# Optimization experiments

Hardware: AMD Instinct MI355X
Metric: run time of the kernel (lower is better)

Reference implementation:

```python
import jax, jax.numpy as jnp
import numpy as np

TIME_STEPS = 49      # time_steps init arg
NUM_STEPS = 5000     # (time_steps+1)/dt = max_solve_steps
DT = 0.01            # dt0 in diffeqsolve
B = 8192             # batch of independent simulations


def setup_inputs() -> dict:
    key = jax.random.key(0)
    k1, k2, k3 = jax.random.split(key, 3)
    # positive, well-conditioned rates in [0.05, 0.5)
    condition = 0.05 + 0.45 * jax.random.uniform(k1, (B, 4), dtype=jnp.float32)
    # standard normals; scaled by sqrt(dt) inside reference -> Brownian increments
    dW = jax.random.normal(k2, (NUM_STEPS, B), dtype=jnp.float32)
    # uniform jitter used in summarize()'s max_at
    u = jax.random.uniform(k3, (B,), dtype=jnp.float32)
    return {"condition": condition, "dW": dW, "u": u}


def _simulate(condition, dW):
    # condition columns: infection_rate, recovery_rate, r0_mean_reversion, r0_volatility
    inf_rate = condition[:, 0]
    rec = condition[:, 1]
    mr = condition[:, 2]
    vol = condition[:, 3]
    r0_init = inf_rate / rec
    b = condition.shape[0]
    y0 = jnp.stack([
        jnp.full((b,), 0.99, condition.dtype),  # S
        jnp.full((b,), 0.01, condition.dtype),  # I
        jnp.zeros((b,), condition.dtype),       # R
        r0_init,                                # R0
    ], axis=-1)  # [B,4]
    sqrt_dt = jnp.sqrt(jnp.asarray(DT, condition.dtype))

    def step(y, dw):
        s, i, r, r0 = y[:, 0], y[:, 1], y[:, 2], y[:, 3]
        newly_infected = r0 * rec * s
        newly_recovered = rec * i
        # Euler-Maruyama: drift * dt + diffusion * dW, diffusion only on R0,
        # scaled by sqrt(|R0|) as in sde()
        y_new = jnp.stack([
            s - DT * newly_infected,
            i + DT * (newly_infected - newly_recovered),
            r + DT * newly_recovered,
            r0 + DT * mr * (r0_init - r0) + jnp.sqrt(jnp.abs(r0)) * vol * (dw * sqrt_dt),
        ], axis=-1)
        return y_new, y_new[:, 1]  # carry full state, emit infected fraction

    _, infected = jax.lax.scan(step, y0, dW)  # infected: [NUM_STEPS, B]
    # SaveAt ts = 1..TIME_STEPS: step k ends at t=(k+1)*DT, so t=m is index 100*m-1
    x = infected[99:100 * TIME_STEPS:100]  # [TIME_STEPS, B]
    return jnp.nan_to_num(x, nan=0.0, posinf=0.0, neginf=0.0)


def reference(condition, dW, u):
    x = _simulate(condition, dW)          # [T, B] infected trajectories
    x = jnp.clip(x, 1e-5)
    max_ = x.max(axis=0)
    max_at = (jnp.argmax(x, axis=0).astype(x.dtype) + u) / TIME_STEPS
    vol = jnp.std(jnp.diff(jnp.log(x), axis=0), axis=0)
    return jnp.stack([max_, max_at, vol], axis=-1)  # [B, 3]
```

## Files before the change

kernel.cpp:

```cpp
#include <hip/hip_runtime.h>
#include <math.h>

#define BATCH 8192
#define TPB   32
#define SEG   50


#define REP50(M) M(0) M(1) M(2) M(3) M(4) M(5) M(6) M(7) M(8) M(9) \
  M(10) M(11) M(12) M(13) M(14) M(15) M(16) M(17) M(18) M(19) \
  M(20) M(21) M(22) M(23) M(24) M(25) M(26) M(27) M(28) M(29) \
  M(30) M(31) M(32) M(33) M(34) M(35) M(36) M(37) M(38) M(39) \
  M(40) M(41) M(42) M(43) M(44) M(45) M(46) M(47) M(48) M(49)

#define DECL_A(k) float A##k = 0.0f;
#define DECL_B(k) float B##k = 0.0f;

#define LDL(k) "global_load_dword %[d" #k "], %[ob], %[sb]\n\t" \
               "v_add_u32 %[ob], 0x8000, %[ob]\n\t"

#define LD25 LDL(0) LDL(1) LDL(2) LDL(3) LDL(4) LDL(5) LDL(6) LDL(7) \
  LDL(8) LDL(9) LDL(10) LDL(11) LDL(12) LDL(13) LDL(14) LDL(15) LDL(16) \
  LDL(17) LDL(18) LDL(19) LDL(20) LDL(21) LDL(22) LDL(23) LDL(24)

#define LOAD_LO(P) asm volatile(LD25 \
  : [d0]"=v"(P##0),[d1]"=v"(P##1),[d2]"=v"(P##2),[d3]"=v"(P##3), \
    [d4]"=v"(P##4),[d5]"=v"(P##5),[d6]"=v"(P##6),[d7]"=v"(P##7), \
    [d8]"=v"(P##8),[d9]"=v"(P##9),[d10]"=v"(P##10),[d11]"=v"(P##11), \
    [d12]"=v"(P##12),[d13]"=v"(P##13),[d14]"=v"(P##14),[d15]"=v"(P##15), \
    [d16]"=v"(P##16),[d17]"=v"(P##17),[d18]"=v"(P##18),[d19]"=v"(P##19), \
    [d20]"=v"(P##20),[d21]"=v"(P##21),[d22]"=v"(P##22),[d23]"=v"(P##23), \
    [d24]"=v"(P##24),[ob]"+v"(ob) \
  : [sb]"s"(dWp))

#define LOAD_HI(P) asm volatile(LD25 \
  : [d0]"=v"(P##25),[d1]"=v"(P##26),[d2]"=v"(P##27),[d3]"=v"(P##28), \
    [d4]"=v"(P##29),[d5]"=v"(P##30),[d6]"=v"(P##31),[d7]"=v"(P##32), \
    [d8]"=v"(P##33),[d9]"=v"(P##34),[d10]"=v"(P##35),[d11]"=v"(P##36), \
    [d12]"=v"(P##37),[d13]"=v"(P##38),[d14]"=v"(P##39),[d15]"=v"(P##40), \
    [d16]"=v"(P##41),[d17]"=v"(P##42),[d18]"=v"(P##43),[d19]"=v"(P##44), \
    [d20]"=v"(P##45),[d21]"=v"(P##46),[d22]"=v"(P##47),[d23]"=v"(P##48), \
    [d24]"=v"(P##49),[ob]"+v"(ob) \
  : [sb]"s"(dWp))

#define WAIT_LO(P) asm volatile("s_waitcnt vmcnt(50)" \
  : "+v"(P##0),"+v"(P##1),"+v"(P##2),"+v"(P##3),"+v"(P##4), \
    "+v"(P##5),"+v"(P##6),"+v"(P##7),"+v"(P##8),"+v"(P##9), \
    "+v"(P##10),"+v"(P##11),"+v"(P##12),"+v"(P##13),"+v"(P##14), \
    "+v"(P##15),"+v"(P##16),"+v"(P##17),"+v"(P##18),"+v"(P##19), \
    "+v"(P##20),"+v"(P##21),"+v"(P##22),"+v"(P##23),"+v"(P##24))

#define WAIT_HI(P) asm volatile("s_waitcnt vmcnt(50)" \
  : "+v"(P##25),"+v"(P##26),"+v"(P##27),"+v"(P##28),"+v"(P##29), \
    "+v"(P##30),"+v"(P##31),"+v"(P##32),"+v"(P##33),"+v"(P##34), \
    "+v"(P##35),"+v"(P##36),"+v"(P##37),"+v"(P##38),"+v"(P##39), \
    "+v"(P##40),"+v"(P##41),"+v"(P##42),"+v"(P##43),"+v"(P##44), \
    "+v"(P##45),"+v"(P##46),"+v"(P##47),"+v"(P##48),"+v"(P##49))

#define STEP_BODY(dwv) { \
    float dw  = (dwv); \
    float pr  = dtrec * r0; \
    float ps  = pr * s; \
    float r0a = r0 * c1 + c2; \
    float sq  = sqrtf(fabsf(r0)); \
    float g   = dw * volc; \
    s  = s - ps; \
    i_ = i_ * ci + ps; \
    r0 = r0a + sq * g; }

#define STEP_A(k) STEP_BODY(A##k)
#define STEP_B(k) STEP_BODY(B##k)

__global__ __attribute__((amdgpu_flat_work_group_size(TPB, TPB),
                          amdgpu_waves_per_eu(1, 1)))
void sir_sde_kernel(const float* __restrict__ cond,
                    const float* __restrict__ dW,
                    const float* __restrict__ uu,
                    float* __restrict__ out)
{
    const int b = blockIdx.x * TPB + threadIdx.x;

    const float u_in     = uu[b];
    const float inf_rate = cond[b * 4 + 0];
    const float rec      = cond[b * 4 + 1];
    const float mr       = cond[b * 4 + 2];
    const float vol      = cond[b * 4 + 3];

    const float dt    = 0.01f;
    const float r0i   = inf_rate / rec;
    const float dtrec = dt * rec;
    const float ci    = 1.0f - dtrec;
    const float c1    = 1.0f - dt * mr;
    const float c2    = (dt * mr) * r0i;
    const float volc  = vol * sqrtf(dt);

    float s  = 0.99f;
    float i_ = 0.01f;
    float r0 = r0i;

    float maxv = -1.0f, maxat = 0.0f;
    float prevlx = 0.0f, sum = 0.0f, sumsq = 0.0f;
    int   reccount = 0;

    REP50(DECL_A)
    REP50(DECL_B)

    const float* dWp = dW;
    unsigned ob = (unsigned)b * 4u;

    LOAD_LO(A); LOAD_HI(A);

#pragma clang loop unroll(disable)
    for (int sg = 0; sg < 98; sg += 2) {
        LOAD_LO(B); LOAD_HI(B);

        WAIT_LO(A); WAIT_HI(A);
        REP50(STEP_A)

        LOAD_LO(A); LOAD_HI(A);

        WAIT_LO(B); WAIT_HI(B);
        REP50(STEP_B)

        {
            float x = __builtin_isfinite(i_) ? i_ : 0.0f;
            x = fmaxf(x, 1e-5f);
            float lx = logf(x);
            if (reccount > 0) {
                float d = lx - prevlx;
                sum   += d;
                sumsq += d * d;
            }
            prevlx = lx;
            if (x > maxv) { maxv = x; maxat = (float)reccount; }
            ++reccount;
        }
    }

    asm volatile("s_waitcnt vmcnt(0)"
      : "+v"(A0),"+v"(A1),"+v"(A2),"+v"(A3),"+v"(A4),"+v"(A5),"+v"(A6),
        "+v"(A7),"+v"(A8),"+v"(A9),"+v"(A10),"+v"(A11),"+v"(A12),"+v"(A13),
        "+v"(A14),"+v"(A15),"+v"(A16),"+v"(A17),"+v"(A18),"+v"(A19),
        "+v"(A20),"+v"(A21),"+v"(A22),"+v"(A23),"+v"(A24) : : "memory");
    asm volatile("s_waitcnt vmcnt(0)"
      : "+v"(A25),"+v"(A26),"+v"(A27),"+v"(A28),"+v"(A29),"+v"(A30),
        "+v"(A31),"+v"(A32),"+v"(A33),"+v"(A34),"+v"(A35),"+v"(A36),
        "+v"(A37),"+v"(A38),"+v"(A39),"+v"(A40),"+v"(A41),"+v"(A42),
        "+v"(A43),"+v"(A44),"+v"(A45),"+v"(A46),"+v"(A47),"+v"(A48),
        "+v"(A49) : : "memory");

    float mean = sum / 48.0f;
    float var  = sumsq / 48.0f - mean * mean;
    var = fmaxf(var, 0.0f);
    float volout    = sqrtf(var);
    float maxat_out = (maxat + u_in) / 49.0f;

    out[b * 3 + 0] = maxv;
    out[b * 3 + 1] = maxat_out;
    out[b * 3 + 2] = volout;
}

extern "C" void kernel_launch(void* const* d_in, const int* in_sizes, int n_in,
                              void* d_out, int out_size, void* d_ws, size_t ws_size,
                              hipStream_t stream)
{
    (void)in_sizes; (void)n_in; (void)out_size; (void)d_ws; (void)ws_size;
    const float* cond = (const float*)d_in[0];
    const float* dW   = (const float*)d_in[1];
    const float* uu   = (const float*)d_in[2];
    float* out = (float*)d_out;

    dim3 grid(BATCH / TPB), block(TPB);
    hipLaunchKernelGGL(sir_sde_kernel, grid, block, 0, stream, cond, dW, uu, out);
}
```

Baseline: 566.8 us.

## Pre-transpose dW into per-block contiguous tiles before the simulation kernel

Adds a reshuffle kernel that rearranges the first 4900 noise rows into a workspace so that each 32-lane block's 50-step segment is one contiguous 6.4KB chunk. The simulation kernel can then use immediate offsets on a fixed lane offset instead of strided 32KB-apart row loads. The aim is better DRAM and TLB locality for the many tiny strided loads. The cost is an extra full read and write pass over about 78MB of dW plus a second launch. The old direct kernel is kept as a fallback when the workspace is too small.

Measured after the change: 613.5 us. 8.2% more time.

```diff
diff --git a/kernel.cpp b/kernel.cpp
--- a/kernel.cpp
+++ b/kernel.cpp
@@ -15,14 +15,60 @@
 #define DECL_A(k) float A##k = 0.0f;
 #define DECL_B(k) float B##k = 0.0f;
 
+#define LD25OFF \
+  "global_load_dword %[d0], %[vo], %[sb]\n\t" \
+  "global_load_dword %[d1], %[vo], %[sb] offset:128\n\t" \
+  "global_load_dword %[d2], %[vo], %[sb] offset:256\n\t" \
+  "global_load_dword %[d3], %[vo], %[sb] offset:384\n\t" \
+  "global_load_dword %[d4], %[vo], %[sb] offset:512\n\t" \
+  "global_load_dword %[d5], %[vo], %[sb] offset:640\n\t" \
+  "global_load_dword %[d6], %[vo], %[sb] offset:768\n\t" \
+  "global_load_dword %[d7], %[vo], %[sb] offset:896\n\t" \
+  "global_load_dword %[d8], %[vo], %[sb] offset:1024\n\t" \
+  "global_load_dword %[d9], %[vo], %[sb] offset:1152\n\t" \
+  "global_load_dword %[d10], %[vo], %[sb] offset:1280\n\t" \
+  "global_load_dword %[d11], %[vo], %[sb] offset:1408\n\t" \
+  "global_load_dword %[d12], %[vo], %[sb] offset:1536\n\t" \
+  "global_load_dword %[d13], %[vo], %[sb] offset:1664\n\t" \
+  "global_load_dword %[d14], %[vo], %[sb] offset:1792\n\t" \
+  "global_load_dword %[d15], %[vo], %[sb] offset:1920\n\t" \
+  "global_load_dword %[d16], %[vo], %[sb] offset:2048\n\t" \
+  "global_load_dword %[d17], %[vo], %[sb] offset:2176\n\t" \
+  "global_load_dword %[d18], %[vo], %[sb] offset:2304\n\t" \
+  "global_load_dword %[d19], %[vo], %[sb] offset:2432\n\t" \
+  "global_load_dword %[d20], %[vo], %[sb] offset:2560\n\t" \
+  "global_load_dword %[d21], %[vo], %[sb] offset:2688\n\t" \
+  "global_load_dword %[d22], %[vo], %[sb] offset:2816\n\t" \
+  "global_load_dword %[d23], %[vo], %[sb] offset:2944\n\t" \
+  "global_load_dword %[d24], %[vo], %[sb] offset:3072"
+
+#define LOAD_LO(P, ptr) asm volatile(LD25OFF \
+  : [d0]"=v"(P##0),[d1]"=v"(P##1),[d2]"=v"(P##2),[d3]"=v"(P##3), \
+    [d4]"=v"(P##4),[d5]"=v"(P##5),[d6]"=v"(P##6),[d7]"=v"(P##7), \
+    [d8]"=v"(P##8),[d9]"=v"(P##9),[d10]"=v"(P##10),[d11]"=v"(P##11), \
+    [d12]"=v"(P##12),[d13]"=v"(P##13),[d14]"=v"(P##14),[d15]"=v"(P##15), \
+    [d16]"=v"(P##16),[d17]"=v"(P##17),[d18]"=v"(P##18),[d19]"=v"(P##19), \
+    [d20]"=v"(P##20),[d21]"=v"(P##21),[d22]"=v"(P##22),[d23]"=v"(P##23), \
+    [d24]"=v"(P##24) \
+  : [vo]"v"(vlane), [sb]"s"(ptr))
+
+#define LOAD_HI(P, ptr) asm volatile(LD25OFF \
+  : [d0]"=v"(P##25),[d1]"=v"(P##26),[d2]"=v"(P##27),[d3]"=v"(P##28), \
+    [d4]"=v"(P##29),[d5]"=v"(P##30),[d6]"=v"(P##31),[d7]"=v"(P##32), \
+    [d8]"=v"(P##33),[d9]"=v"(P##34),[d10]"=v"(P##35),[d11]"=v"(P##36), \
+    [d12]"=v"(P##37),[d13]"=v"(P##38),[d14]"=v"(P##39),[d15]"=v"(P##40), \
+    [d16]"=v"(P##41),[d17]"=v"(P##42),[d18]"=v"(P##43),[d19]"=v"(P##44), \
+    [d20]"=v"(P##45),[d21]"=v"(P##46),[d22]"=v"(P##47),[d23]"=v"(P##48), \
+    [d24]"=v"(P##49) \
+  : [vo]"v"(vlane), [sb]"s"(ptr))
+
 #define LDL(k) "global_load_dword %[d" #k "], %[ob], %[sb]\n\t" \
                "v_add_u32 %[ob], 0x8000, %[ob]\n\t"
-
-#define LD25 LDL(0) LDL(1) LDL(2) LDL(3) LDL(4) LDL(5) LDL(6) LDL(7) \
+#define LD25B LDL(0) LDL(1) LDL(2) LDL(3) LDL(4) LDL(5) LDL(6) LDL(7) \
   LDL(8) LDL(9) LDL(10) LDL(11) LDL(12) LDL(13) LDL(14) LDL(15) LDL(16) \
   LDL(17) LDL(18) LDL(19) LDL(20) LDL(21) LDL(22) LDL(23) LDL(24)
 
-#define LOAD_LO(P) asm volatile(LD25 \
+#define LOADD_LO(P) asm volatile(LD25B \
   : [d0]"=v"(P##0),[d1]"=v"(P##1),[d2]"=v"(P##2),[d3]"=v"(P##3), \
     [d4]"=v"(P##4),[d5]"=v"(P##5),[d6]"=v"(P##6),[d7]"=v"(P##7), \
     [d8]"=v"(P##8),[d9]"=v"(P##9),[d10]"=v"(P##10),[d11]"=v"(P##11), \
@@ -31,8 +77,7 @@
     [d20]"=v"(P##20),[d21]"=v"(P##21),[d22]"=v"(P##22),[d23]"=v"(P##23), \
     [d24]"=v"(P##24),[ob]"+v"(ob) \
   : [sb]"s"(dWp))
-
-#define LOAD_HI(P) asm volatile(LD25 \
+#define LOADD_HI(P) asm volatile(LD25B \
   : [d0]"=v"(P##25),[d1]"=v"(P##26),[d2]"=v"(P##27),[d3]"=v"(P##28), \
     [d4]"=v"(P##29),[d5]"=v"(P##30),[d6]"=v"(P##31),[d7]"=v"(P##32), \
     [d8]"=v"(P##33),[d9]"=v"(P##34),[d10]"=v"(P##35),[d11]"=v"(P##36), \
@@ -48,7 +93,6 @@
     "+v"(P##10),"+v"(P##11),"+v"(P##12),"+v"(P##13),"+v"(P##14), \
     "+v"(P##15),"+v"(P##16),"+v"(P##17),"+v"(P##18),"+v"(P##19), \
     "+v"(P##20),"+v"(P##21),"+v"(P##22),"+v"(P##23),"+v"(P##24))
-
 #define WAIT_HI(P) asm volatile("s_waitcnt vmcnt(50)" \
   : "+v"(P##25),"+v"(P##26),"+v"(P##27),"+v"(P##28),"+v"(P##29), \
     "+v"(P##30),"+v"(P##31),"+v"(P##32),"+v"(P##33),"+v"(P##34), \
@@ -70,105 +114,155 @@
 #define STEP_A(k) STEP_BODY(A##k)
 #define STEP_B(k) STEP_BODY(B##k)
 
+#define SIM_PROLOG \
+    const int bx = blockIdx.x; \
+    const int lane = threadIdx.x; \
+    const int b = bx * TPB + lane; \
+    const float u_in     = uu[b]; \
+    const float inf_rate = cond[b * 4 + 0]; \
+    const float rec      = cond[b * 4 + 1]; \
+    const float mr       = cond[b * 4 + 2]; \
+    const float vol      = cond[b * 4 + 3]; \
+    const float dt    = 0.01f; \
+    const float r0i   = inf_rate / rec; \
+    const float dtrec = dt * rec; \
+    const float ci    = 1.0f - dtrec; \
+    const float c1    = 1.0f - dt * mr; \
+    const float c2    = (dt * mr) * r0i; \
+    const float volc  = vol * sqrtf(dt); \
+    float s  = 0.99f; \
+    float i_ = 0.01f; \
+    float r0 = r0i; \
+    float maxv = -1.0f, maxat = 0.0f; \
+    float prevlx = 0.0f, sum = 0.0f, sumsq = 0.0f; \
+    int   reccount = 0; \
+    REP50(DECL_A) \
+    REP50(DECL_B)
+
+#define RECORD_BLOCK { \
+    float x = __builtin_isfinite(i_) ? i_ : 0.0f; \
+    x = fmaxf(x, 1e-5f); \
+    float lx = logf(x); \
+    if (reccount > 0) { float d = lx - prevlx; sum += d; sumsq += d * d; } \
+    prevlx = lx; \
+    if (x > maxv) { maxv = x; maxat = (float)reccount; } \
+    ++reccount; }
+
+#define SIM_EPILOG \
+    asm volatile("s_waitcnt vmcnt(0)" \
+      : "+v"(A0),"+v"(A1),"+v"(A2),"+v"(A3),"+v"(A4),"+v"(A5),"+v"(A6), \
+        "+v"(A7),"+v"(A8),"+v"(A9),"+v"(A10),"+v"(A11),"+v"(A12),"+v"(A13), \
+        "+v"(A14),"+v"(A15),"+v"(A16),"+v"(A17),"+v"(A18),"+v"(A19), \
+        "+v"(A20),"+v"(A21),"+v"(A22),"+v"(A23),"+v"(A24) : : "memory"); \
+    asm volatile("s_waitcnt vmcnt(0)" \
+      : "+v"(A25),"+v"(A26),"+v"(A27),"+v"(A28),"+v"(A29),"+v"(A30), \
+        "+v"(A31),"+v"(A32),"+v"(A33),"+v"(A34),"+v"(A35),"+v"(A36), \
+        "+v"(A37),"+v"(A38),"+v"(A39),"+v"(A40),"+v"(A41),"+v"(A42), \
+        "+v"(A43),"+v"(A44),"+v"(A45),"+v"(A46),"+v"(A47),"+v"(A48), \
+        "+v"(A49) : : "memory"); \
+    float mean = sum / 48.0f; \
+    float var  = sumsq / 48.0f - mean * mean; \
+    var = fmaxf(var, 0.0f); \
+    out[b * 3 + 0] = maxv; \
+    out[b * 3 + 1] = (maxat + u_in) / 49.0f; \
+    out[b * 3 + 2] = sqrtf(var);
+
+__global__ __launch_bounds__(256)
+void reshuffle_kernel(const float* __restrict__ src, float* __restrict__ dst)
+{
+    const unsigned t  = blockIdx.x * 256u + threadIdx.x;
+    const unsigned e4 = t * 4u;
+    const unsigned row = e4 >> 13;
+    const unsigned b0  = e4 & 8191u;
+    const unsigned sg  = row / 50u;
+    const unsigned r   = row - sg * 50u;
+    const unsigned bx  = b0 >> 5;
+    const unsigned i0  = b0 & 31u;
+    const float4 v = ((const float4*)src)[t];
+    const unsigned dst4 = ((sg * 256u + bx) * 50u + r) * 8u + (i0 >> 2);
+    ((float4*)dst)[dst4] = v;
+}
+
 __global__ __attribute__((amdgpu_flat_work_group_size(TPB, TPB),
                           amdgpu_waves_per_eu(1, 1)))
-void sir_sde_kernel(const float* __restrict__ cond,
+void sir_sde_reshuf(const float* __restrict__ cond,
+                    const float* __restrict__ dWr,
+                    const float* __restrict__ uu,
+                    float* __restrict__ out)
+{
+    SIM_PROLOG
+    const unsigned vlane = (unsigned)lane * 4u;
+
+    const float* pA0 = dWr + (size_t)bx * 1600;
+    LOAD_LO(A, pA0); LOAD_HI(A, pA0 + 800);
+
+#pragma clang loop unroll(disable)
+    for (int sg = 0; sg < 98; sg += 2) {
+        const float* pB = dWr + ((size_t)(sg + 1) * 256 + bx) * 1600;
+        LOAD_LO(B, pB); LOAD_HI(B, pB + 800);
+
+        WAIT_LO(A); WAIT_HI(A);
+        REP50(STEP_A)
+
+        const int nxt = (sg + 2 < 98) ? (sg + 2) : 0;
+        const float* pA = dWr + ((size_t)nxt * 256 + bx) * 1600;
+        LOAD_LO(A, pA); LOAD_HI(A, pA + 800);
+
+        WAIT_LO(B); WAIT_HI(B);
+        REP50(STEP_B)
+
+        RECORD_BLOCK
+    }
+
+    SIM_EPILOG
+}
+
+__global__ __attribute__((amdgpu_flat_work_group_size(TPB, TPB),
+                          amdgpu_waves_per_eu(1, 1)))
+void sir_sde_direct(const float* __restrict__ cond,
                     const float* __restrict__ dW,
                     const float* __restrict__ uu,
                     float* __restrict__ out)
 {
-    const int b = blockIdx.x * TPB + threadIdx.x;
-
-    const float u_in     = uu[b];
-    const float inf_rate = cond[b * 4 + 0];
-    const float rec      = cond[b * 4 + 1];
-    const float mr       = cond[b * 4 + 2];
-    const float vol      = cond[b * 4 + 3];
-
-    const float dt    = 0.01f;
-    const float r0i   = inf_rate / rec;
-    const float dtrec = dt * rec;
-    const float ci    = 1.0f - dtrec;
-    const float c1    = 1.0f - dt * mr;
-    const float c2    = (dt * mr) * r0i;
-    const float volc  = vol * sqrtf(dt);
-
-    float s  = 0.99f;
-    float i_ = 0.01f;
-    float r0 = r0i;
-
-    float maxv = -1.0f, maxat = 0.0f;
-    float prevlx = 0.0f, sum = 0.0f, sumsq = 0.0f;
-    int   reccount = 0;
-
-    REP50(DECL_A)
-    REP50(DECL_B)
-
+    SIM_PROLOG
     const float* dWp = dW;
     unsigned ob = (unsigned)b * 4u;
 
-    LOAD_LO(A); LOAD_HI(A);
+    LOADD_LO(A); LOADD_HI(A);
 
 #pragma clang loop unroll(disable)
     for (int sg = 0; sg < 98; sg += 2) {
-        LOAD_LO(B); LOAD_HI(B);
-
+        LOADD_LO(B); LOADD_HI(B);
         WAIT_LO(A); WAIT_HI(A);
         REP50(STEP_A)
-
-        LOAD_LO(A); LOAD_HI(A);
-
+        LOADD_LO(A); LOADD_HI(A);
         WAIT_LO(B); WAIT_HI(B);
         REP50(STEP_B)
-
-        {
-            float x = __builtin_isfinite(i_) ? i_ : 0.0f;
-            x = fmaxf(x, 1e-5f);
-            float lx = logf(x);
-            if (reccount > 0) {
-                float d = lx - prevlx;
-                sum   += d;
-                sumsq += d * d;
-            }
-            prevlx = lx;
-            if (x > maxv) { maxv = x; maxat = (float)reccount; }
-            ++reccount;
-        }
+        RECORD_BLOCK
     }
 
-    asm volatile("s_waitcnt vmcnt(0)"
-      : "+v"(A0),"+v"(A1),"+v"(A2),"+v"(A3),"+v"(A4),"+v"(A5),"+v"(A6),
-        "+v"(A7),"+v"(A8),"+v"(A9),"+v"(A10),"+v"(A11),"+v"(A12),"+v"(A13),
-        "+v"(A14),"+v"(A15),"+v"(A16),"+v"(A17),"+v"(A18),"+v"(A19),
-        "+v"(A20),"+v"(A21),"+v"(A22),"+v"(A23),"+v"(A24) : : "memory");
-    asm volatile("s_waitcnt vmcnt(0)"
-      : "+v"(A25),"+v"(A26),"+v"(A27),"+v"(A28),"+v"(A29),"+v"(A30),
-        "+v"(A31),"+v"(A32),"+v"(A33),"+v"(A34),"+v"(A35),"+v"(A36),
-        "+v"(A37),"+v"(A38),"+v"(A39),"+v"(A40),"+v"(A41),"+v"(A42),
-        "+v"(A43),"+v"(A44),"+v"(A45),"+v"(A46),"+v"(A47),"+v"(A48),
-        "+v"(A49) : : "memory");
-
-    float mean = sum / 48.0f;
-    float var  = sumsq / 48.0f - mean * mean;
-    var = fmaxf(var, 0.0f);
-    float volout    = sqrtf(var);
-    float maxat_out = (maxat + u_in) / 49.0f;
-
-    out[b * 3 + 0] = maxv;
-    out[b * 3 + 1] = maxat_out;
-    out[b * 3 + 2] = volout;
+    SIM_EPILOG
 }
 
 extern "C" void kernel_launch(void* const* d_in, const int* in_sizes, int n_in,
                               void* d_out, int out_size, void* d_ws, size_t ws_size,
                               hipStream_t stream)
 {
-    (void)in_sizes; (void)n_in; (void)out_size; (void)d_ws; (void)ws_size;
+    (void)in_sizes; (void)n_in; (void)out_size;
     const float* cond = (const float*)d_in[0];
     const float* dW   = (const float*)d_in[1];
     const float* uu   = (const float*)d_in[2];
     float* out = (float*)d_out;
 
-    dim3 grid(BATCH / TPB), block(TPB);
-    hipLaunchKernelGGL(sir_sde_kernel, grid, block, 0, stream, cond, dW, uu, out);
-}
+    const size_t need = (size_t)4900 * 8192 * 4;
+    if (ws_size >= need) {
+        float* dWr = (float*)d_ws;
+        hipLaunchKernelGGL(reshuffle_kernel, dim3(4900u * 8192u / 4u / 256u),
+                           dim3(256), 0, stream, dW, dWr);
+        hipLaunchKernelGGL(sir_sde_reshuf, dim3(BATCH / TPB), dim3(TPB), 0,
+                           stream, cond, dWr, uu, out);
+    } else {
+        hipLaunchKernelGGL(sir_sde_direct, dim3(BATCH / TPB), dim3(TPB), 0,
+                           stream, cond, dW, uu, out);
+    }
+}
```

## Reshuffle dW into per-block segments and stream via LDS DMA with producer waves

Applied to the files above, without the earlier changes.

Adds a pre-pass kernel that reorders the needed 4900 rows of dW into contiguous per-block, per-segment chunks in the workspace. The main kernel then uses 256-thread blocks where three waves issue global_load_lds DMA into a 4-deep LDS ring while one wave runs the serial SDE recurrence, reading 4 steps at a time as float4. This is meant to take long-latency strided global loads off the compute wave's critical path. In exchange it costs an extra full pass over dW (read plus write), a second launch, and per-step barriers. The old direct kernel is kept as a fallback for when the workspace is too small.

Measured after the change: 600.6 us. 6.0% more time.

```diff
diff --git a/kernel.cpp b/kernel.cpp
--- a/kernel.cpp
+++ b/kernel.cpp
@@ -2,59 +2,12 @@
 #include <math.h>
 
 #define BATCH 8192
-#define TPB   32
-#define SEG   50
-
-
-#define REP50(M) M(0) M(1) M(2) M(3) M(4) M(5) M(6) M(7) M(8) M(9) \
-  M(10) M(11) M(12) M(13) M(14) M(15) M(16) M(17) M(18) M(19) \
-  M(20) M(21) M(22) M(23) M(24) M(25) M(26) M(27) M(28) M(29) \
-  M(30) M(31) M(32) M(33) M(34) M(35) M(36) M(37) M(38) M(39) \
-  M(40) M(41) M(42) M(43) M(44) M(45) M(46) M(47) M(48) M(49)
-
-#define DECL_A(k) float A##k = 0.0f;
-#define DECL_B(k) float B##k = 0.0f;
-
-#define LDL(k) "global_load_dword %[d" #k "], %[ob], %[sb]\n\t" \
-               "v_add_u32 %[ob], 0x8000, %[ob]\n\t"
-
-#define LD25 LDL(0) LDL(1) LDL(2) LDL(3) LDL(4) LDL(5) LDL(6) LDL(7) \
-  LDL(8) LDL(9) LDL(10) LDL(11) LDL(12) LDL(13) LDL(14) LDL(15) LDL(16) \
-  LDL(17) LDL(18) LDL(19) LDL(20) LDL(21) LDL(22) LDL(23) LDL(24)
-
-#define LOAD_LO(P) asm volatile(LD25 \
-  : [d0]"=v"(P##0),[d1]"=v"(P##1),[d2]"=v"(P##2),[d3]"=v"(P##3), \
-    [d4]"=v"(P##4),[d5]"=v"(P##5),[d6]"=v"(P##6),[d7]"=v"(P##7), \
-    [d8]"=v"(P##8),[d9]"=v"(P##9),[d10]"=v"(P##10),[d11]"=v"(P##11), \
-    [d12]"=v"(P##12),[d13]"=v"(P##13),[d14]"=v"(P##14),[d15]"=v"(P##15), \
-    [d16]"=v"(P##16),[d17]"=v"(P##17),[d18]"=v"(P##18),[d19]"=v"(P##19), \
-    [d20]"=v"(P##20),[d21]"=v"(P##21),[d22]"=v"(P##22),[d23]"=v"(P##23), \
-    [d24]"=v"(P##24),[ob]"+v"(ob) \
-  : [sb]"s"(dWp))
-
-#define LOAD_HI(P) asm volatile(LD25 \
-  : [d0]"=v"(P##25),[d1]"=v"(P##26),[d2]"=v"(P##27),[d3]"=v"(P##28), \
-    [d4]"=v"(P##29),[d5]"=v"(P##30),[d6]"=v"(P##31),[d7]"=v"(P##32), \
-    [d8]"=v"(P##33),[d9]"=v"(P##34),[d10]"=v"(P##35),[d11]"=v"(P##36), \
-    [d12]"=v"(P##37),[d13]"=v"(P##38),[d14]"=v"(P##39),[d15]"=v"(P##40), \
-    [d16]"=v"(P##41),[d17]"=v"(P##42),[d18]"=v"(P##43),[d19]"=v"(P##44), \
-    [d20]"=v"(P##45),[d21]"=v"(P##46),[d22]"=v"(P##47),[d23]"=v"(P##48), \
-    [d24]"=v"(P##49),[ob]"+v"(ob) \
-  : [sb]"s"(dWp))
-
-#define WAIT_LO(P) asm volatile("s_waitcnt vmcnt(50)" \
-  : "+v"(P##0),"+v"(P##1),"+v"(P##2),"+v"(P##3),"+v"(P##4), \
-    "+v"(P##5),"+v"(P##6),"+v"(P##7),"+v"(P##8),"+v"(P##9), \
-    "+v"(P##10),"+v"(P##11),"+v"(P##12),"+v"(P##13),"+v"(P##14), \
-    "+v"(P##15),"+v"(P##16),"+v"(P##17),"+v"(P##18),"+v"(P##19), \
-    "+v"(P##20),"+v"(P##21),"+v"(P##22),"+v"(P##23),"+v"(P##24))
-
-#define WAIT_HI(P) asm volatile("s_waitcnt vmcnt(50)" \
-  : "+v"(P##25),"+v"(P##26),"+v"(P##27),"+v"(P##28),"+v"(P##29), \
-    "+v"(P##30),"+v"(P##31),"+v"(P##32),"+v"(P##33),"+v"(P##34), \
-    "+v"(P##35),"+v"(P##36),"+v"(P##37),"+v"(P##38),"+v"(P##39), \
-    "+v"(P##40),"+v"(P##41),"+v"(P##42),"+v"(P##43),"+v"(P##44), \
-    "+v"(P##45),"+v"(P##46),"+v"(P##47),"+v"(P##48),"+v"(P##49))
+#define TPB_FB 32
+
+
+typedef float f4v __attribute__((ext_vector_type(4)));
+typedef __attribute__((address_space(1))) const void gas_v;
+typedef __attribute__((address_space(3))) void las_v;
 
 #define STEP_BODY(dwv) { \
     float dw  = (dwv); \
@@ -67,108 +20,229 @@
     i_ = i_ * ci + ps; \
     r0 = r0a + sq * g; }
 
-#define STEP_A(k) STEP_BODY(A##k)
-#define STEP_B(k) STEP_BODY(B##k)
-
-__global__ __attribute__((amdgpu_flat_work_group_size(TPB, TPB),
+#define RECORD_BLOCK { \
+    float x = __builtin_isfinite(i_) ? i_ : 0.0f; \
+    x = fmaxf(x, 1e-5f); \
+    float lx = logf(x); \
+    if (reccount > 0) { float d = lx - prevlx; sum += d; sumsq += d * d; } \
+    prevlx = lx; \
+    if (x > maxv) { maxv = x; maxat = (float)reccount; } \
+    ++reccount; }
+
+#define SIM_CONSTS \
+    const float dt    = 0.01f; \
+    const float r0i   = inf_rate / rec; \
+    const float dtrec = dt * rec; \
+    const float ci    = 1.0f - dtrec; \
+    const float c1    = 1.0f - dt * mr; \
+    const float c2    = (dt * mr) * r0i; \
+    const float volc  = vol * sqrtf(dt); \
+    float s  = 0.99f; \
+    float i_ = 0.01f; \
+    float r0 = r0i; \
+    float maxv = -1.0f, maxat = 0.0f; \
+    float prevlx = 0.0f, sum = 0.0f, sumsq = 0.0f; \
+    int   reccount = 0;
+
+__global__ __launch_bounds__(256)
+void reshuffle_x4(const float* __restrict__ src, float* __restrict__ dst)
+{
+    const unsigned t  = blockIdx.x * 256u + threadIdx.x;
+    const unsigned i  = t & 31u;
+    const unsigned r1 = t >> 5;
+    const unsigned rg = r1 % 25u;
+    const unsigned r2 = r1 / 25u;
+    const unsigned bx = r2 & 255u;
+    const unsigned sl = r2 >> 8;
+    const unsigned seg = 48u - sl;
+    const unsigned row0 = seg * 100u + rg * 4u;
+    const unsigned bcol = bx * 32u + i;
+    f4v v;
+    v.x = src[(size_t)(row0 + 0) * BATCH + bcol];
+    v.y = src[(size_t)(row0 + 1) * BATCH + bcol];
+    v.z = src[(size_t)(row0 + 2) * BATCH + bcol];
+    v.w = src[(size_t)(row0 + 3) * BATCH + bcol];
+    const size_t dst4 = ((size_t)(seg * 256u + bx) * 25u + rg) * 32u + i;
+    ((f4v*)dst)[dst4] = v;
+}
+
+__device__ __forceinline__ void dma_seg(const float* reg, float* lb, int l64)
+{
+#pragma unroll
+    for (int j = 0; j < 12; ++j)
+        __builtin_amdgcn_global_load_lds((gas_v*)(reg + j * 256 + l64 * 4),
+                                         (las_v*)(lb + j * 256), 16, 0, 0);
+    if (l64 < 32)
+        __builtin_amdgcn_global_load_lds((gas_v*)(reg + 3072 + l64 * 4),
+                                         (las_v*)(lb + 3072), 16, 0, 0);
+}
+
+__global__ __attribute__((amdgpu_flat_work_group_size(256, 256),
                           amdgpu_waves_per_eu(1, 1)))
-void sir_sde_kernel(const float* __restrict__ cond,
-                    const float* __restrict__ dW,
-                    const float* __restrict__ uu,
-                    float* __restrict__ out)
-{
-    const int b = blockIdx.x * TPB + threadIdx.x;
+void sir_sde_lds(const float* __restrict__ cond,
+                 const float* __restrict__ dWr,
+                 const float* __restrict__ uu,
+                 float* __restrict__ out)
+{
+    __shared__ __align__(16) float sbuf[4][3200];
+
+    const int bx   = blockIdx.x;
+    const int lane = threadIdx.x & 31;
+    const int l64  = threadIdx.x & 63;
+    const int wv   = threadIdx.x >> 6;
+    const int b    = bx * 32 + lane;
 
     const float u_in     = uu[b];
     const float inf_rate = cond[b * 4 + 0];
     const float rec      = cond[b * 4 + 1];
     const float mr       = cond[b * 4 + 2];
     const float vol      = cond[b * 4 + 3];
-
-    const float dt    = 0.01f;
-    const float r0i   = inf_rate / rec;
-    const float dtrec = dt * rec;
-    const float ci    = 1.0f - dtrec;
-    const float c1    = 1.0f - dt * mr;
-    const float c2    = (dt * mr) * r0i;
-    const float volc  = vol * sqrtf(dt);
-
-    float s  = 0.99f;
-    float i_ = 0.01f;
-    float r0 = r0i;
-
-    float maxv = -1.0f, maxat = 0.0f;
-    float prevlx = 0.0f, sum = 0.0f, sumsq = 0.0f;
-    int   reccount = 0;
-
-    REP50(DECL_A)
-    REP50(DECL_B)
-
+    SIM_CONSTS
+
+    const size_t regstride = 3200;
+
+    if (wv == 1) dma_seg(dWr + ((size_t)0 * 256 + bx) * regstride, sbuf[0], l64);
+    if (wv == 2) dma_seg(dWr + ((size_t)1 * 256 + bx) * regstride, sbuf[1], l64);
+    if (wv == 1 || wv == 2)
+        asm volatile("s_waitcnt vmcnt(0)" ::: "memory");
+    __syncthreads();
+
+#pragma clang loop unroll(disable)
+    for (int k = 0; k < 49; ++k) {
+        if (k + 1 <= 48 && wv == 1 + (k + 1) % 3)
+            asm volatile("s_waitcnt vmcnt(0)" ::: "memory");
+        asm volatile("s_barrier" ::: "memory");
+
+        if (k + 2 <= 48 && wv == 1 + (k + 2) % 3)
+            dma_seg(dWr + ((size_t)(k + 2) * 256 + bx) * regstride,
+                    sbuf[(k + 2) & 3], l64);
+
+        if (threadIdx.x < 32) {
+            const float* sb = sbuf[k & 3];
+#pragma unroll
+            for (int j = 0; j < 25; ++j) {
+                const f4v d = *(const f4v*)(sb + j * 128 + lane * 4);
+                STEP_BODY(d.x) STEP_BODY(d.y) STEP_BODY(d.z) STEP_BODY(d.w)
+            }
+            RECORD_BLOCK
+        }
+    }
+
+    if (threadIdx.x < 32) {
+        float mean = sum / 48.0f;
+        float var  = sumsq / 48.0f - mean * mean;
+        var = fmaxf(var, 0.0f);
+        out[b * 3 + 0] = maxv;
+        out[b * 3 + 1] = (maxat + u_in) / 49.0f;
+        out[b * 3 + 2] = sqrtf(var);
+    }
+}
+
+#define REP50(M) M(0) M(1) M(2) M(3) M(4) M(5) M(6) M(7) M(8) M(9) \
+  M(10) M(11) M(12) M(13) M(14) M(15) M(16) M(17) M(18) M(19) \
+  M(20) M(21) M(22) M(23) M(24) M(25) M(26) M(27) M(28) M(29) \
+  M(30) M(31) M(32) M(33) M(34) M(35) M(36) M(37) M(38) M(39) \
+  M(40) M(41) M(42) M(43) M(44) M(45) M(46) M(47) M(48) M(49)
+#define DECL_a(k) float a##k = 0.0f;
+#define DECL_b(k) float b##k = 0.0f;
+#define LDL(k) "global_load_dword %[d" #k "], %[ob], %[sb]\n\t" \
+               "v_add_u32 %[ob], 0x8000, %[ob]\n\t"
+#define LD25B LDL(0) LDL(1) LDL(2) LDL(3) LDL(4) LDL(5) LDL(6) LDL(7) \
+  LDL(8) LDL(9) LDL(10) LDL(11) LDL(12) LDL(13) LDL(14) LDL(15) LDL(16) \
+  LDL(17) LDL(18) LDL(19) LDL(20) LDL(21) LDL(22) LDL(23) LDL(24)
+#define LOADD_LO(P) asm volatile(LD25B \
+  : [d0]"=v"(P##0),[d1]"=v"(P##1),[d2]"=v"(P##2),[d3]"=v"(P##3), \
+    [d4]"=v"(P##4),[d5]"=v"(P##5),[d6]"=v"(P##6),[d7]"=v"(P##7), \
+    [d8]"=v"(P##8),[d9]"=v"(P##9),[d10]"=v"(P##10),[d11]"=v"(P##11), \
+    [d12]"=v"(P##12),[d13]"=v"(P##13),[d14]"=v"(P##14),[d15]"=v"(P##15), \
+    [d16]"=v"(P##16),[d17]"=v"(P##17),[d18]"=v"(P##18),[d19]"=v"(P##19), \
+    [d20]"=v"(P##20),[d21]"=v"(P##21),[d22]"=v"(P##22),[d23]"=v"(P##23), \
+    [d24]"=v"(P##24),[ob]"+v"(ob) \
+  : [sb]"s"(dWp))
+#define LOADD_HI(P) asm volatile(LD25B \
+  : [d0]"=v"(P##25),[d1]"=v"(P##26),[d2]"=v"(P##27),[d3]"=v"(P##28), \
+    [d4]"=v"(P##29),[d5]"=v"(P##30),[d6]"=v"(P##31),[d7]"=v"(P##32), \
+    [d8]"=v"(P##33),[d9]"=v"(P##34),[d10]"=v"(P##35),[d11]"=v"(P##36), \
+    [d12]"=v"(P##37),[d13]"=v"(P##38),[d14]"=v"(P##39),[d15]"=v"(P##40), \
+    [d16]"=v"(P##41),[d17]"=v"(P##42),[d18]"=v"(P##43),[d19]"=v"(P##44), \
+    [d20]"=v"(P##45),[d21]"=v"(P##46),[d22]"=v"(P##47),[d23]"=v"(P##48), \
+    [d24]"=v"(P##49),[ob]"+v"(ob) \
+  : [sb]"s"(dWp))
+#define WAIT_LO(P) asm volatile("s_waitcnt vmcnt(50)" \
+  : "+v"(P##0),"+v"(P##1),"+v"(P##2),"+v"(P##3),"+v"(P##4), \
+    "+v"(P##5),"+v"(P##6),"+v"(P##7),"+v"(P##8),"+v"(P##9), \
+    "+v"(P##10),"+v"(P##11),"+v"(P##12),"+v"(P##13),"+v"(P##14), \
+    "+v"(P##15),"+v"(P##16),"+v"(P##17),"+v"(P##18),"+v"(P##19), \
+    "+v"(P##20),"+v"(P##21),"+v"(P##22),"+v"(P##23),"+v"(P##24))
+#define WAIT_HI(P) asm volatile("s_waitcnt vmcnt(50)" \
+  : "+v"(P##25),"+v"(P##26),"+v"(P##27),"+v"(P##28),"+v"(P##29), \
+    "+v"(P##30),"+v"(P##31),"+v"(P##32),"+v"(P##33),"+v"(P##34), \
+    "+v"(P##35),"+v"(P##36),"+v"(P##37),"+v"(P##38),"+v"(P##39), \
+    "+v"(P##40),"+v"(P##41),"+v"(P##42),"+v"(P##43),"+v"(P##44), \
+    "+v"(P##45),"+v"(P##46),"+v"(P##47),"+v"(P##48),"+v"(P##49))
+#define STEP_a(k) STEP_BODY(a##k)
+#define STEP_b(k) STEP_BODY(b##k)
+
+__global__ __attribute__((amdgpu_flat_work_group_size(TPB_FB, TPB_FB),
+                          amdgpu_waves_per_eu(1, 1)))
+void sir_sde_direct(const float* __restrict__ cond,
+                    const float* __restrict__ dW,
+                    const float* __restrict__ uu,
+                    float* __restrict__ out)
+{
+    const int bx   = blockIdx.x;
+    const int lane = threadIdx.x;
+    const int b    = bx * TPB_FB + lane;
+    const float u_in     = uu[b];
+    const float inf_rate = cond[b * 4 + 0];
+    const float rec      = cond[b * 4 + 1];
+    const float mr       = cond[b * 4 + 2];
+    const float vol      = cond[b * 4 + 3];
+    SIM_CONSTS
+    REP50(DECL_a)
+    REP50(DECL_b)
     const float* dWp = dW;
     unsigned ob = (unsigned)b * 4u;
 
-    LOAD_LO(A); LOAD_HI(A);
-
+    LOADD_LO(a); LOADD_HI(a);
 #pragma clang loop unroll(disable)
     for (int sg = 0; sg < 98; sg += 2) {
-        LOAD_LO(B); LOAD_HI(B);
-
-        WAIT_LO(A); WAIT_HI(A);
-        REP50(STEP_A)
-
-        LOAD_LO(A); LOAD_HI(A);
-
-        WAIT_LO(B); WAIT_HI(B);
-        REP50(STEP_B)
-
-        {
-            float x = __builtin_isfinite(i_) ? i_ : 0.0f;
-            x = fmaxf(x, 1e-5f);
-            float lx = logf(x);
-            if (reccount > 0) {
-                float d = lx - prevlx;
-                sum   += d;
-                sumsq += d * d;
-            }
-            prevlx = lx;
-            if (x > maxv) { maxv = x; maxat = (float)reccount; }
-            ++reccount;
-        }
-    }
-
-    asm volatile("s_waitcnt vmcnt(0)"
-      : "+v"(A0),"+v"(A1),"+v"(A2),"+v"(A3),"+v"(A4),"+v"(A5),"+v"(A6),
-        "+v"(A7),"+v"(A8),"+v"(A9),"+v"(A10),"+v"(A11),"+v"(A12),"+v"(A13),
-        "+v"(A14),"+v"(A15),"+v"(A16),"+v"(A17),"+v"(A18),"+v"(A19),
-        "+v"(A20),"+v"(A21),"+v"(A22),"+v"(A23),"+v"(A24) : : "memory");
-    asm volatile("s_waitcnt vmcnt(0)"
-      : "+v"(A25),"+v"(A26),"+v"(A27),"+v"(A28),"+v"(A29),"+v"(A30),
-        "+v"(A31),"+v"(A32),"+v"(A33),"+v"(A34),"+v"(A35),"+v"(A36),
-        "+v"(A37),"+v"(A38),"+v"(A39),"+v"(A40),"+v"(A41),"+v"(A42),
-        "+v"(A43),"+v"(A44),"+v"(A45),"+v"(A46),"+v"(A47),"+v"(A48),
-        "+v"(A49) : : "memory");
-
+        LOADD_LO(b); LOADD_HI(b);
+        WAIT_LO(a); WAIT_HI(a);
+        REP50(STEP_a)
+        LOADD_LO(a); LOADD_HI(a);
+        WAIT_LO(b); WAIT_HI(b);
+        REP50(STEP_b)
+        RECORD_BLOCK
+    }
+    asm volatile("s_waitcnt vmcnt(0)" ::: "memory");
     float mean = sum / 48.0f;
     float var  = sumsq / 48.0f - mean * mean;
     var = fmaxf(var, 0.0f);
-    float volout    = sqrtf(var);
-    float maxat_out = (maxat + u_in) / 49.0f;
-
     out[b * 3 + 0] = maxv;
-    out[b * 3 + 1] = maxat_out;
-    out[b * 3 + 2] = volout;
+    out[b * 3 + 1] = (maxat + u_in) / 49.0f;
+    out[b * 3 + 2] = sqrtf(var);
 }
 
 extern "C" void kernel_launch(void* const* d_in, const int* in_sizes, int n_in,
                               void* d_out, int out_size, void* d_ws, size_t ws_size,
                               hipStream_t stream)
 {
-    (void)in_sizes; (void)n_in; (void)out_size; (void)d_ws; (void)ws_size;
+    (void)in_sizes; (void)n_in; (void)out_size;
     const float* cond = (const float*)d_in[0];
     const float* dW   = (const float*)d_in[1];
     const float* uu   = (const float*)d_in[2];
     float* out = (float*)d_out;
 
-    dim3 grid(BATCH / TPB), block(TPB);
-    hipLaunchKernelGGL(sir_sde_kernel, grid, block, 0, stream, cond, dW, uu, out);
-}
+    const size_t need = (size_t)4900 * BATCH * 4;
+    if (ws_size >= need) {
+        float* dWr = (float*)d_ws;
+        hipLaunchKernelGGL(reshuffle_x4, dim3(39200), dim3(256), 0, stream,
+                           dW, dWr);
+        hipLaunchKernelGGL(sir_sde_lds, dim3(256), dim3(256), 0, stream,
+                           cond, dWr, uu, out);
+    } else {
+        hipLaunchKernelGGL(sir_sde_direct, dim3(BATCH / TPB_FB), dim3(TPB_FB),
+                           0, stream, cond, dW, uu, out);
+    }
+}
```
